# Kernel optimization log

Measured on AMD Instinct MI355X. Metric: run time of the kernel, lower is better.

## Reference

```python
import jax, jax.numpy as jnp
import numpy as np

B, L, D = 2, 2048, 2048
H, HKV, HD = 16, 4, 128
GROUPS = H // HKV


def _rope_tables(key):
    # standard RoPE cos/sin tables, shape (B, L, HD)
    inv_freq = 1.0 / (10000.0 ** (jnp.arange(0, HD, 2, dtype=jnp.float32) / HD))
    pos = jnp.arange(L, dtype=jnp.float32)
    freqs = pos[:, None] * inv_freq[None, :]          # (L, HD/2)
    emb = jnp.concatenate([freqs, freqs], axis=-1)    # (L, HD)
    cos = jnp.broadcast_to(jnp.cos(emb)[None], (B, L, HD))
    sin = jnp.broadcast_to(jnp.sin(emb)[None], (B, L, HD))
    return cos, sin


def setup_inputs() -> dict:
    key = jax.random.key(0)
    ks = jax.random.split(key, 5)
    x = jax.random.normal(ks[0], (B, L, D), dtype=jnp.float32)
    cos, sin = _rope_tables(ks[1])
    s = 1.0 / np.sqrt(D)
    Wq = jax.random.normal(ks[2], (D, D), dtype=jnp.float32) * s
    bq = jnp.zeros((D,), dtype=jnp.float32)
    Wkv = jax.random.normal(ks[3], (2 * HKV * HD, D), dtype=jnp.float32) * s
    bkv = jnp.zeros((2 * HKV * HD,), dtype=jnp.float32)
    Wo = jax.random.normal(ks[4], (D, D), dtype=jnp.float32) * s
    bo = jnp.zeros((D,), dtype=jnp.float32)
    return {"x": x, "cos": cos, "sin": sin, "Wq": Wq, "bq": bq,
            "Wkv": Wkv, "bkv": bkv, "Wo": Wo, "bo": bo}


def _rotate_half(t):
    t1, t2 = jnp.split(t, 2, axis=-1)
    return jnp.concatenate([-t2, t1], axis=-1)


def reference(x, cos, sin, Wq, bq, Wkv, bkv, Wo, bo):
    b, l, d = x.shape
    # QKV projections
    q = (x @ Wq.T + bq).reshape(b, l, H, HD)
    kv = (x @ Wkv.T + bkv).reshape(b, l, 2, HKV, HD)
    k, v = kv[:, :, 0], kv[:, :, 1]
    # RoPE (unsqueeze over head dim, layout B,L,H,D)
    c = cos[:, :, None, :]
    s = sin[:, :, None, :]
    q = q * c + _rotate_half(q) * s
    k = k * c + _rotate_half(k) * s
    # GQA: expand kv heads to query heads
    k = jnp.repeat(k, GROUPS, axis=2)
    v = jnp.repeat(v, GROUPS, axis=2)
    # causal attention (flash_attn_func equivalent math)
    scores = jnp.einsum("blhd,bmhd->bhlm", q, k) / jnp.sqrt(jnp.float32(HD))
    mask = jnp.tril(jnp.ones((l, l), dtype=bool))
    scores = jnp.where(mask[None, None], scores, jnp.finfo(scores.dtype).min)
    attn = jax.nn.softmax(scores, axis=-1)
    out = jnp.einsum("bhlm,bmhd->blhd", attn, v).reshape(b, l, H * HD)
    return out @ Wo.T + bo
```

## Files before the change

kernel.cpp:

```cpp
#include <hip/hip_runtime.h>
#include <hip/hip_bf16.h>
#include <cstddef>

constexpr int B = 2, L = 2048, D = 2048;
constexpr int H = 16, HKV = 4, HD = 128;
constexpr int GROUPS = H / HKV;
constexpr int KVD = 2 * HKV * HD;
constexpr int M_ROWS = B * L;
constexpr int QKVW = D + KVD;

typedef __attribute__((ext_vector_type(8))) short short8;
typedef __attribute__((ext_vector_type(4))) short s16x4;
typedef __attribute__((ext_vector_type(4))) float f32x4;

__device__ __forceinline__ short f2bf(float f) {
    union { float f; unsigned u; } v; v.f = f;
    unsigned r = v.u + 0x7FFFu + ((v.u >> 16) & 1u);
    return (short)(r >> 16);
}

__device__ __forceinline__ float fast_exp2(float x) {
#if __has_builtin(__builtin_amdgcn_exp2f)
    return __builtin_amdgcn_exp2f(x);
#else
    return exp2f(x);
#endif
}

__device__ __forceinline__ int invp(int pos) {
    const int b16 = pos >> 4, j = pos & 15;
    return ((b16 >> 1) << 4) + j + ((b16 & 1) << 6);
}

typedef __attribute__((address_space(1))) const void cg_void;
typedef __attribute__((address_space(3))) void lds_void;
__device__ __forceinline__ void gl_lds16(const void* g, void* l) {
    __builtin_amdgcn_global_load_lds((cg_void*)g, (lds_void*)l, 16, 0, 0);
}

__global__ __launch_bounds__(256) void cast_all(
    const float* __restrict__ x, const float* __restrict__ Wq,
    const float* __restrict__ Wkv, const float* __restrict__ Wo,
    short* __restrict__ xb, short* __restrict__ wqkvb, short* __restrict__ wob)
{
    constexpr int n_x   = M_ROWS * D / 4;
    constexpr int n_wq  = D * D / 4;
    constexpr int n_wkv = KVD * D / 4;
    constexpr int RPW   = D / 4;
    int i = blockIdx.x * 256 + threadIdx.x;
    const float* src; short* dst; int isrc;
    if (i < n_x) {
        src = x; dst = xb; isrc = i;
    } else if (i < n_x + n_wq) {
        i -= n_x; src = Wq; dst = wqkvb;
        const int fi = i / RPW, col = i % RPW;
        const int head = fi >> 7, pos = fi & 127;
        isrc = ((head << 7) + invp(pos)) * RPW + col;
    } else if (i < n_x + n_wq + n_wkv) {
        i -= n_x + n_wq; src = Wkv; dst = wqkvb + (size_t)D * D;
        const int fi = i / RPW, col = i % RPW;
        if (fi < HKV * HD) {
            isrc = (((fi >> 7) << 7) + invp(fi & 127)) * RPW + col;
        } else {
            isrc = i;
        }
    } else {
        i -= n_x + n_wq + n_wkv; src = Wo; dst = wob; isrc = i;
    }
    const float4 f = ((const float4*)src)[isrc];
    s16x4 s;
    s[0] = f2bf(f.x); s[1] = f2bf(f.y); s[2] = f2bf(f.z); s[3] = f2bf(f.w);
    ((s16x4*)dst)[i] = s;
}

__global__ __launch_bounds__(256) void bcat(
    const float* __restrict__ bq, const float* __restrict__ bkv, float* __restrict__ o)
{
    const int i = blockIdx.x * 256 + threadIdx.x;
    float v;
    if (i < D)                  v = bq[((i >> 7) << 7) + invp(i & 127)];
    else if (i < D + HKV * HD)  v = bkv[(((i - D) >> 7) << 7) + invp((i - D) & 127)];
    else                        v = bkv[i - D];
    o[i] = v;
}

template<int MODE>
__global__ __launch_bounds__(512, 2) void gemm256(
    const short* __restrict__ Ag, const short* __restrict__ Wg,
    const float* __restrict__ bias, float* __restrict__ C,
    const float* __restrict__ cosp, const float* __restrict__ sinp,
    short* __restrict__ qout, short* __restrict__ kout, short* __restrict__ vtout,
    int M, int N, int K)
{
    __shared__ __align__(1024) char smem[131072];

    const int tid = threadIdx.x;
    const int w = tid >> 6, lane = tid & 63;
    const int quad = lane >> 4, n16 = lane & 15;
    const int wr = w >> 2, wc = w & 3;

    const int nbx = gridDim.x;
    const int nwg = nbx * gridDim.y;
    int wg = blockIdx.y * nbx + blockIdx.x;
    wg = (wg & 7) * (nwg >> 3) + (wg >> 3);
    const int bm = (wg / nbx) << 8;
    const int bn = (wg % nbx) << 8;

    const int nkt = K >> 6;

    const int sbo = n16 * 64 + ((quad * 16) ^ ((n16 & 8) << 2));

    const int srow = lane >> 2;
    const int scol = ((lane & 3) * 8) ^ (((lane >> 5) & 1) << 4);

    f32x4 acc[8][4];
#pragma unroll
    for (int i = 0; i < 8; ++i)
#pragma unroll
        for (int j = 0; j < 4; ++j)
#pragma unroll
            for (int r = 0; r < 4; ++r) acc[i][j][r] = 0.f;

    short8 afr[4][2], bfr[2][2];

#define STAGE_A(k0, cb, h)                                                     \
    { _Pragma("unroll") for (int j = 0; j < 2; ++j) {                          \
        const int s  = w + j * 8;                                              \
        const int u  = s >> 1;                                                 \
        const int rg = ((u >> 2) << 3) + ((h) << 2) + (u & 3);                 \
        const int gr = bm + (rg << 4) + srow;                                  \
        const int gc = (k0) + ((s & 1) << 5) + scol;                           \
        gl_lds16(Ag + (size_t)gr * K + gc,                                     \
                 smem + (cb) * 32768 + (h) * 16384 + (s << 10)); } }

#define STAGE_B(k0, cb, h)                                                     \
    { _Pragma("unroll") for (int j = 0; j < 2; ++j) {                          \
        const int s  = w + j * 8;                                              \
        const int u  = s >> 1;                                                 \
        const int rg = ((u >> 1) << 2) + ((h) << 1) + (u & 1);                 \
        const int gr = bn + (rg << 4) + srow;                                  \
        const int gc = (k0) + ((s & 1) << 5) + scol;                           \
        gl_lds16(Wg + (size_t)gr * K + gc,                                     \
                 smem + 65536 + (cb) * 32768 + (h) * 16384 + (s << 10)); } }

#define PHASE(CB, Q, STAGE_STMT, WAIT_STMT)                                    \
    {                                                                          \
        if (((Q) & 1) == 0) {                                                  \
            _Pragma("unroll") for (int mi2 = 0; mi2 < 4; ++mi2)                \
            _Pragma("unroll") for (int kk = 0; kk < 2; ++kk)                   \
                afr[mi2][kk] = *(const short8*)(smem + (CB) * 32768 +          \
                    ((Q) >> 1) * 16384 +                                       \
                    ((((wr * 4 + mi2) * 2) + kk) << 10) + sbo);                \
        }                                                                      \
        _Pragma("unroll") for (int ni2 = 0; ni2 < 2; ++ni2)                    \
        _Pragma("unroll") for (int kk = 0; kk < 2; ++kk)                       \
            bfr[ni2][kk] = *(const short8*)(smem + 65536 + (CB) * 32768 +      \
                ((Q) & 1) * 16384 +                                            \
                ((((wc * 2 + ni2) * 2) + kk) << 10) + sbo);                    \
        STAGE_STMT;                                                            \
        WAIT_STMT;                                                             \
        __builtin_amdgcn_s_barrier();                                          \
        asm volatile("s_waitcnt lgkmcnt(0)" ::: "memory");                     \
        __builtin_amdgcn_sched_barrier(0);                                     \
        __builtin_amdgcn_s_setprio(1);                                         \
        _Pragma("unroll") for (int mi2 = 0; mi2 < 4; ++mi2)                    \
        _Pragma("unroll") for (int ni2 = 0; ni2 < 2; ++ni2)                    \
        _Pragma("unroll") for (int kk = 0; kk < 2; ++kk)                       \
            acc[((Q) >> 1) * 4 + mi2][((Q) & 1) * 2 + ni2] =                   \
                __builtin_amdgcn_mfma_f32_16x16x32_bf16(                       \
                    afr[mi2][kk], bfr[ni2][kk],                                \
                    acc[((Q) >> 1) * 4 + mi2][((Q) & 1) * 2 + ni2], 0, 0, 0);  \
        __builtin_amdgcn_s_setprio(0);                                         \
        asm volatile("" ::: "memory");                                         \
        __builtin_amdgcn_s_barrier();                                          \
    }

#define NOP_WAIT asm volatile("" ::: "memory")

    STAGE_A(0, 0, 0);
    STAGE_B(0, 0, 0);
    STAGE_A(0, 0, 1);
    STAGE_B(0, 0, 1);
    if (nkt > 1) {
        STAGE_A(64, 1, 0);
        STAGE_B(64, 1, 0);
    }
    asm volatile("s_waitcnt vmcnt(4)" ::: "memory");
    __builtin_amdgcn_s_barrier();

    for (int t = 0; t < nkt; t += 2) {
        const int k1 = (t + 1) << 6, k2 = (t + 2) << 6, k3 = (t + 3) << 6;
        const bool g2 = (t + 2) < nkt, g3 = (t + 3) < nkt;

        PHASE(0, 0, { STAGE_A(k1, 1, 1); }, NOP_WAIT);
        PHASE(0, 1, { STAGE_B(k1, 1, 1); }, NOP_WAIT);
        PHASE(0, 2, { if (g2) STAGE_A(k2, 0, 0); }, NOP_WAIT);
        PHASE(0, 3, { if (g2) STAGE_B(k2, 0, 0); },
              { if (g2) asm volatile("s_waitcnt vmcnt(4)" ::: "memory");
                else    asm volatile("s_waitcnt vmcnt(0)" ::: "memory"); });

        PHASE(1, 0, { if (g2) STAGE_A(k2, 0, 1); }, NOP_WAIT);
        PHASE(1, 1, { if (g2) STAGE_B(k2, 0, 1); }, NOP_WAIT);
        PHASE(1, 2, { if (g3) STAGE_A(k3, 1, 0); }, NOP_WAIT);
        PHASE(1, 3, { if (g3) STAGE_B(k3, 1, 0); },
              { if (g3) asm volatile("s_waitcnt vmcnt(4)" ::: "memory");
                else    asm volatile("s_waitcnt vmcnt(0)" ::: "memory"); });
    }

#undef PHASE
#undef STAGE_A
#undef STAGE_B
#undef NOP_WAIT

    if (MODE == 0) {
#pragma unroll
        for (int mh = 0; mh < 2; ++mh)
#pragma unroll
            for (int mi2 = 0; mi2 < 4; ++mi2)
#pragma unroll
                for (int r = 0; r < 4; ++r) {
                    const int row = bm + wr * 128 + mh * 64 + mi2 * 16 + quad * 4 + r;
#pragma unroll
                    for (int nh = 0; nh < 2; ++nh)
#pragma unroll
                        for (int ni2 = 0; ni2 < 2; ++ni2) {
                            const int col = bn + wc * 64 + nh * 32 + ni2 * 16 + n16;
                            C[(size_t)row * N + col] =
                                acc[mh * 4 + mi2][nh * 2 + ni2][r] + bias[col];
                        }
                }
    } else {
        short* const T = (short*)smem;
        __syncthreads();
        if (bn < D + HKV * HD) {
#pragma unroll
            for (int mh = 0; mh < 2; ++mh)
#pragma unroll
                for (int mi2 = 0; mi2 < 4; ++mi2)
#pragma unroll
                    for (int r = 0; r < 4; ++r) {
                        const int rl = wr * 128 + mh * 64 + mi2 * 16 + quad * 4 + r;
                        const int row = bm + rl;
                        const float* csrow = cosp + (size_t)row * HD;
                        const float* snrow = sinp + (size_t)row * HD;
                        const int sw = ((rl >> 2) & 7) << 4;
#pragma unroll
                        for (int nh = 0; nh < 2; ++nh) {
                            const int cl = wc * 64 + nh * 32 + n16;
                            const int iif = (wc & 1) * 32 + nh * 16 + n16;
                            const float a  = acc[mh * 4 + mi2][nh * 2 + 0][r] + bias[bn + cl];
                            const float bb = acc[mh * 4 + mi2][nh * 2 + 1][r] + bias[bn + cl + 16];
                            const float olo = a * csrow[iif]       - bb * snrow[iif];
                            const float ohi = bb * csrow[iif + 64] + a * snrow[iif + 64];
                            *(short*)((char*)T + ((rl * 512 + cl * 2) ^ sw))        = f2bf(olo);
                            *(short*)((char*)T + ((rl * 512 + (cl + 16) * 2) ^ sw)) = f2bf(ohi);
                        }
                    }
            __syncthreads();
            const bool isK = (bn >= D);
#pragma unroll
            for (int it = 0; it < 16; ++it) {
                const int idx = it * 512 + tid;
                const int rl = idx >> 5, c8 = idx & 31;
                const short8 v = *(const short8*)((char*)T +
                    ((rl * 512 + c8 * 16) ^ (((rl >> 2) & 7) << 4)));
                const int row = bm + rl;
                if (!isK) {
                    *(short8*)&qout[(size_t)row * D + bn + c8 * 8] = v;
                } else {
                    const int ck = bn - D + c8 * 8;
                    const int hk = ck >> 7, dk = ck & 127;
                    const int b_ = row >> 11, l_ = row & (L - 1);
                    *(short8*)&kout[((size_t)(b_ * HKV + hk) * L + l_) * HD + dk] = v;
                }
            }
        } else {
#pragma unroll
            for (int mh = 0; mh < 2; ++mh)
#pragma unroll
                for (int mi2 = 0; mi2 < 4; ++mi2) {
                    const int l0 = wr * 128 + mh * 64 + mi2 * 16 + quad * 4;
#pragma unroll
                    for (int nh = 0; nh < 2; ++nh)
#pragma unroll
                        for (int ni2 = 0; ni2 < 2; ++ni2) {
                            const int cl = wc * 64 + nh * 32 + ni2 * 16 + n16;
                            const float bs = bias[bn + cl];
                            s16x4 sv;
#pragma unroll
                            for (int r = 0; r < 4; ++r)
                                sv[r] = f2bf(acc[mh * 4 + mi2][nh * 2 + ni2][r] + bs);
                            *(s16x4*)((char*)T + ((cl * 512 + l0 * 2) ^ ((cl & 7) << 4))) = sv;
                        }
                }
            __syncthreads();
#pragma unroll
            for (int it = 0; it < 16; ++it) {
                const int idx = it * 512 + tid;
                const int cvr = idx >> 5, l8 = idx & 31;
                const short8 v = *(const short8*)((char*)T +
                    ((cvr * 512 + l8 * 16) ^ ((cvr & 7) << 4)));
                const int cv = bn - (D + HKV * HD) + cvr;
                const int hv = cv >> 7, dv = cv & 127;
                const int b_ = bm >> 11;
                const int lg = (bm & (L - 1)) + l8 * 8;
                *(short8*)&vtout[((size_t)(b_ * HKV + hv) * HD + dv) * L + lg] = v;
            }
        }
    }
}

__global__ __launch_bounds__(512) void attn_mfma4(
    const short* __restrict__ qb_, const short* __restrict__ kb_,
    const short* __restrict__ vtb_, short* __restrict__ ob)
{
    __shared__ __align__(16) char smem[86016];
    short* const KsB  = (short*)smem;
    short* const VtB  = (short*)(smem + 32768);
    short* const PbB  = (short*)(smem + 65536);
    float* const Rbuf = (float*)smem;

    const int hkv = blockIdx.y, b = blockIdx.z;
    const int tid = threadIdx.x;
    const int w = tid >> 6, lane = tid & 63;
    const int quad = lane >> 4, n16 = lane & 15;
    const int h   = hkv * GROUPS + (w & 3);
    const int kh  = (w >> 2) * 32;
    const int khg = (w >> 2) * 4;

    const size_t kbase  = (size_t)(b * HKV + hkv) * L * HD;
    const size_t vtbase = (size_t)(b * HKV + hkv) * HD * L;
    const float c1 = 0.12751845f;
    const float c0 = -28.853901f;

    short8 ones;
#pragma unroll
    for (int i = 0; i < 8; ++i) ones[i] = (short)0x3F80;

    const int kr = lane >> 4;
    const int kg_sw = lane & 15;
    const int vr = lane >> 3;
    const int vg_sw = lane & 7;

    short* const myPb = PbB + w * (2 * 16 * 40);

#pragma unroll 1
    for (int phase = 0; phase < 2; ++phase) {
        const int qidx = phase ? (63 - (int)blockIdx.x) : (int)blockIdx.x;
        const int qb0 = qidx * 32;
        const int ntiles = (qidx >> 1) + 1;

        short8 qf[2][4];
#pragma unroll
        for (int rt = 0; rt < 2; ++rt)
#pragma unroll
            for (int kk = 0; kk < 4; ++kk)
                qf[rt][kk] = *(const short8*)&qb_[
                    ((size_t)(b * L + qb0 + rt * 16 + n16)) * D + h * HD + kk * 32 + quad * 8];

        f32x4 oacc[2][8], lacc[2];
#pragma unroll
        for (int rt = 0; rt < 2; ++rt) {
#pragma unroll
            for (int r = 0; r < 4; ++r) lacc[rt][r] = 0.f;
#pragma unroll
            for (int nt = 0; nt < 8; ++nt)
#pragma unroll
                for (int r = 0; r < 4; ++r) oacc[rt][nt][r] = 0.f;
        }

        __syncthreads();

        {
            const short* kg = kb_ + kbase;
            const short* vg = vtb_ + vtbase;
#pragma unroll
            for (int j = 0; j < 2; ++j) {
                const int chunk = w * 2 + j;
                const int r = chunk * 4 + kr;
                gl_lds16(kg + r * HD + (kg_sw ^ (r & 15)) * 8, KsB + chunk * 512);
            }
#pragma unroll
            for (int j = 0; j < 2; ++j) {
                const int chunk = w * 2 + j;
                const int d = chunk * 8 + vr;
                gl_lds16(vg + (size_t)d * L + (vg_sw ^ (d & 7)) * 8, VtB + chunk * 512);
            }
        }

        for (int kt = 0; kt < ntiles; ++kt) {
            const int buf = kt & 1;
            __syncthreads();

            if (kt + 1 < ntiles) {
                const short* kg = kb_ + kbase + (size_t)((kt + 1) * 64) * HD;
                const short* vg = vtb_ + vtbase + (kt + 1) * 64;
#pragma unroll
                for (int j = 0; j < 2; ++j) {
                    const int chunk = w * 2 + j;
                    const int r = chunk * 4 + kr;
                    gl_lds16(kg + r * HD + (kg_sw ^ (r & 15)) * 8,
                             KsB + (buf ^ 1) * 8192 + chunk * 512);
                }
#pragma unroll
                for (int j = 0; j < 2; ++j) {
                    const int chunk = w * 2 + j;
                    const int d = chunk * 8 + vr;
                    gl_lds16(vg + (size_t)d * L + (vg_sw ^ (d & 7)) * 8,
                             VtB + (buf ^ 1) * 8192 + chunk * 512);
                }
            }

            const short* Ks = KsB + buf * 8192;
            const short* Vt = VtB + buf * 8192;

            f32x4 s[2][2];
#pragma unroll
            for (int rt = 0; rt < 2; ++rt)
#pragma unroll
                for (int ktl = 0; ktl < 2; ++ktl)
#pragma unroll
                    for (int r = 0; r < 4; ++r) s[rt][ktl][r] = 0.f;
#pragma unroll
            for (int kk = 0; kk < 4; ++kk) {
                short8 kf[2];
#pragma unroll
                for (int ktl = 0; ktl < 2; ++ktl) {
                    const int row = kh + ktl * 16 + n16;
                    kf[ktl] = *(const short8*)&Ks[row * 128 + ((kk * 4 + quad) ^ n16) * 8];
                }
#pragma unroll
                for (int rt = 0; rt < 2; ++rt)
#pragma unroll
                    for (int ktl = 0; ktl < 2; ++ktl)
                        s[rt][ktl] = __builtin_amdgcn_mfma_f32_16x16x32_bf16(
                            qf[rt][kk], kf[ktl], s[rt][ktl], 0, 0, 0);
            }

            const bool lastt = (kt == ntiles - 1);
#pragma unroll
            for (int rt = 0; rt < 2; ++rt) {
#pragma unroll
                for (int ktl = 0; ktl < 2; ++ktl) {
                    const int key0 = kt * 64 + kh + ktl * 16 + n16;
#pragma unroll
                    for (int r = 0; r < 4; ++r) {
                        float sv = s[rt][ktl][r];
                        if (lastt) {
                            const int qi = qb0 + rt * 16 + quad * 4 + r;
                            sv = (key0 <= qi) ? sv : -1e30f;
                        }
                        const float e = fast_exp2(sv * c1 + c0);
                        myPb[(rt * 16 + quad * 4 + r) * 40 + ktl * 16 + n16] = f2bf(e);
                    }
                }
            }
            asm volatile("s_waitcnt lgkmcnt(0)" ::: "memory");

            short8 pf[2];
#pragma unroll
            for (int rt = 0; rt < 2; ++rt)
                pf[rt] = *(const short8*)&myPb[(rt * 16 + n16) * 40 + quad * 8];
#pragma unroll
            for (int rt = 0; rt < 2; ++rt)
                lacc[rt] = __builtin_amdgcn_mfma_f32_16x16x32_bf16(pf[rt], ones, lacc[rt], 0, 0, 0);
#pragma unroll
            for (int nt = 0; nt < 8; ++nt) {
                const short8 vf = *(const short8*)&Vt[
                    (nt * 16 + n16) * 64 + ((khg + quad) ^ (n16 & 7)) * 8];
#pragma unroll
                for (int rt = 0; rt < 2; ++rt)
                    oacc[rt][nt] = __builtin_amdgcn_mfma_f32_16x16x32_bf16(pf[rt], vf, oacc[rt][nt], 0, 0, 0);
            }
        }

        __syncthreads();
        if (w >= 4) {
            float* rp = Rbuf + ((size_t)(w - 4) * 64 + lane) * 76;
#pragma unroll
            for (int rt = 0; rt < 2; ++rt)
#pragma unroll
                for (int nt = 0; nt < 8; ++nt)
                    *(f32x4*)&rp[(rt * 8 + nt) * 4] = oacc[rt][nt];
            *(f32x4*)&rp[64] = lacc[0];
            *(f32x4*)&rp[68] = lacc[1];
        }
        __syncthreads();
        if (w < 4) {
            const float* rp = Rbuf + ((size_t)w * 64 + lane) * 76;
#pragma unroll
            for (int rt = 0; rt < 2; ++rt) {
                const f32x4 lr = *(const f32x4*)&rp[64 + rt * 4];
#pragma unroll
                for (int r = 0; r < 4; ++r) lacc[rt][r] += lr[r];
#pragma unroll
                for (int nt = 0; nt < 8; ++nt) {
                    const f32x4 o2 = *(const f32x4*)&rp[(rt * 8 + nt) * 4];
#pragma unroll
                    for (int r = 0; r < 4; ++r) oacc[rt][nt][r] += o2[r];
                }
            }
#pragma unroll
            for (int rt = 0; rt < 2; ++rt) {
#pragma unroll
                for (int r = 0; r < 4; ++r) {
                    const float inv = 1.0f / lacc[rt][r];
                    short* op = ob + ((size_t)(b * L + qb0 + rt * 16 + quad * 4 + r)) * D + h * HD + n16;
#pragma unroll
                    for (int nt = 0; nt < 8; ++nt) op[nt * 16] = f2bf(oacc[rt][nt][r] * inv);
                }
            }
        }
    }
}

extern "C" void kernel_launch(void* const* d_in, const int* in_sizes, int n_in,
                              void* d_out, int out_size, void* d_ws, size_t ws_size,
                              hipStream_t stream)
{
    const float* x    = (const float*)d_in[0];
    const float* cosp = (const float*)d_in[1];
    const float* sinp = (const float*)d_in[2];
    const float* Wq   = (const float*)d_in[3];
    const float* bq   = (const float*)d_in[4];
    const float* Wkv  = (const float*)d_in[5];
    const float* bkv  = (const float*)d_in[6];
    const float* Wo   = (const float*)d_in[7];
    const float* bo   = (const float*)d_in[8];
    float* out = (float*)d_out;

    char* p = (char*)d_ws;
    short* x_bf    = (short*)p; p += (size_t)M_ROWS * D * 2;
    short* wqkv_bf = (short*)p; p += (size_t)QKVW * D * 2;
    short* wo_bf   = (short*)p; p += (size_t)D * D * 2;
    float* b_qkv   = (float*)p; p += (size_t)QKVW * 4;
    short* q_bf    = (short*)p; p += (size_t)M_ROWS * D * 2;
    short* k_bf    = (short*)p; p += (size_t)M_ROWS * HKV * HD * 2;
    short* vt_bf   = (short*)p;
    short* attn_bf = x_bf;

    dim3 blk(256);

    cast_all<<<dim3(18432), blk, 0, stream>>>(x, Wq, Wkv, Wo, x_bf, wqkv_bf, wo_bf);
    bcat<<<dim3(QKVW / 256), blk, 0, stream>>>(bq, bkv, b_qkv);

    gemm256<1><<<dim3(QKVW / 256, M_ROWS / 256), dim3(512), 0, stream>>>(
        x_bf, wqkv_bf, b_qkv, nullptr, cosp, sinp, q_bf, k_bf, vt_bf,
        M_ROWS, QKVW, D);

    attn_mfma4<<<dim3(32, HKV, B), dim3(512), 0, stream>>>(q_bf, k_bf, vt_bf, attn_bf);

    gemm256<0><<<dim3(D / 256, M_ROWS / 256), dim3(512), 0, stream>>>(
        attn_bf, wo_bf, bo, out, nullptr, nullptr, nullptr, nullptr, nullptr,
        M_ROWS, D, D);
}
```

Measured before the change: 303.1 us.

## Fold bias concat into cast kernel and halve GEMM phases per K-tile

The separate bias-concatenation kernel is removed and its work moved into extra threads of the cast kernel, saving one launch. The GEMM main loop drops from four phases per K-tile to two: each phase loads a full 4x4 fragment set (B fragments read once per tile), issues 32 MFMAs and stages A and B together. This halves barriers per tile and cuts redundant LDS reads, but uses more B-fragment registers and issues larger bursts of global loads at once, which can lower overlap or occupancy.

```diff
diff --git a/kernel.cpp b/kernel.cpp
--- a/kernel.cpp
+++ b/kernel.cpp
@@ -41,13 +41,32 @@
 __global__ __launch_bounds__(256) void cast_all(
     const float* __restrict__ x, const float* __restrict__ Wq,
     const float* __restrict__ Wkv, const float* __restrict__ Wo,
-    short* __restrict__ xb, short* __restrict__ wqkvb, short* __restrict__ wob)
+    const float* __restrict__ bq, const float* __restrict__ bkv,
+    short* __restrict__ xb, short* __restrict__ wqkvb, short* __restrict__ wob,
+    float* __restrict__ bqkv)
 {
     constexpr int n_x   = M_ROWS * D / 4;
     constexpr int n_wq  = D * D / 4;
     constexpr int n_wkv = KVD * D / 4;
+    constexpr int n_wo  = D * D / 4;
+    constexpr int n_w   = n_x + n_wq + n_wkv + n_wo;
     constexpr int RPW   = D / 4;
     int i = blockIdx.x * 256 + threadIdx.x;
+    if (i >= n_w) {
+        const int j = i - n_w;
+        float4 o;
+#pragma unroll
+        for (int e = 0; e < 4; ++e) {
+            const int idx = j * 4 + e;
+            float v;
+            if (idx < D)                 v = bq[((idx >> 7) << 7) + invp(idx & 127)];
+            else if (idx < D + HKV * HD) v = bkv[(((idx - D) >> 7) << 7) + invp((idx - D) & 127)];
+            else                         v = bkv[idx - D];
+            (&o.x)[e] = v;
+        }
+        ((float4*)bqkv)[j] = o;
+        return;
+    }
     const float* src; short* dst; int isrc;
     if (i < n_x) {
         src = x; dst = xb; isrc = i;
@@ -73,17 +92,6 @@
     ((s16x4*)dst)[i] = s;
 }
 
-__global__ __launch_bounds__(256) void bcat(
-    const float* __restrict__ bq, const float* __restrict__ bkv, float* __restrict__ o)
-{
-    const int i = blockIdx.x * 256 + threadIdx.x;
-    float v;
-    if (i < D)                  v = bq[((i >> 7) << 7) + invp(i & 127)];
-    else if (i < D + HKV * HD)  v = bkv[(((i - D) >> 7) << 7) + invp((i - D) & 127)];
-    else                        v = bkv[i - D];
-    o[i] = v;
-}
-
 template<int MODE>
 __global__ __launch_bounds__(512, 2) void gemm256(
     const short* __restrict__ Ag, const short* __restrict__ Wg,
@@ -121,7 +129,7 @@
 #pragma unroll
             for (int r = 0; r < 4; ++r) acc[i][j][r] = 0.f;
 
-    short8 afr[4][2], bfr[2][2];
+    short8 afr[4][2], bfr[4][2];
 
 #define STAGE_A(k0, cb, h)                                                     \
     { _Pragma("unroll") for (int j = 0; j < 2; ++j) {                          \
@@ -143,20 +151,19 @@
         gl_lds16(Wg + (size_t)gr * K + gc,                                     \
                  smem + 65536 + (cb) * 32768 + (h) * 16384 + (s << 10)); } }
 
-#define PHASE(CB, Q, STAGE_STMT, WAIT_STMT)                                    \
+#define PHASE(CB, MH, RDB, STAGE_STMT, WAIT_STMT)                              \
     {                                                                          \
-        if (((Q) & 1) == 0) {                                                  \
-            _Pragma("unroll") for (int mi2 = 0; mi2 < 4; ++mi2)                \
+        if (RDB) {                                                             \
+            _Pragma("unroll") for (int nj = 0; nj < 4; ++nj)                   \
             _Pragma("unroll") for (int kk = 0; kk < 2; ++kk)                   \
-                afr[mi2][kk] = *(const short8*)(smem + (CB) * 32768 +          \
-                    ((Q) >> 1) * 16384 +                                       \
-                    ((((wr * 4 + mi2) * 2) + kk) << 10) + sbo);                \
+                bfr[nj][kk] = *(const short8*)(smem + 65536 + (CB) * 32768 +   \
+                    (nj >> 1) * 16384 +                                        \
+                    ((((wc * 2 + (nj & 1)) * 2) + kk) << 10) + sbo);           \
         }                                                                      \
-        _Pragma("unroll") for (int ni2 = 0; ni2 < 2; ++ni2)                    \
+        _Pragma("unroll") for (int mi2 = 0; mi2 < 4; ++mi2)                    \
         _Pragma("unroll") for (int kk = 0; kk < 2; ++kk)                       \
-            bfr[ni2][kk] = *(const short8*)(smem + 65536 + (CB) * 32768 +      \
-                ((Q) & 1) * 16384 +                                            \
-                ((((wc * 2 + ni2) * 2) + kk) << 10) + sbo);                    \
+            afr[mi2][kk] = *(const short8*)(smem + (CB) * 32768 +              \
+                (MH) * 16384 + ((((wr * 4 + mi2) * 2) + kk) << 10) + sbo);     \
         STAGE_STMT;                                                            \
         WAIT_STMT;                                                             \
         __builtin_amdgcn_s_barrier();                                          \
@@ -164,12 +171,12 @@
         __builtin_amdgcn_sched_barrier(0);                                     \
         __builtin_amdgcn_s_setprio(1);                                         \
         _Pragma("unroll") for (int mi2 = 0; mi2 < 4; ++mi2)                    \
-        _Pragma("unroll") for (int ni2 = 0; ni2 < 2; ++ni2)                    \
+        _Pragma("unroll") for (int nj = 0; nj < 4; ++nj)                       \
         _Pragma("unroll") for (int kk = 0; kk < 2; ++kk)                       \
-            acc[((Q) >> 1) * 4 + mi2][((Q) & 1) * 2 + ni2] =                   \
+            acc[(MH) * 4 + mi2][nj] =                                          \
                 __builtin_amdgcn_mfma_f32_16x16x32_bf16(                       \
-                    afr[mi2][kk], bfr[ni2][kk],                                \
-                    acc[((Q) >> 1) * 4 + mi2][((Q) & 1) * 2 + ni2], 0, 0, 0);  \
+                    afr[mi2][kk], bfr[nj][kk], acc[(MH) * 4 + mi2][nj],        \
+                    0, 0, 0);                                                  \
         __builtin_amdgcn_s_setprio(0);                                         \
         asm volatile("" ::: "memory");                                         \
         __builtin_amdgcn_s_barrier();                                          \
@@ -184,25 +191,23 @@
     if (nkt > 1) {
         STAGE_A(64, 1, 0);
         STAGE_B(64, 1, 0);
-    }
-    asm volatile("s_waitcnt vmcnt(4)" ::: "memory");
+        asm volatile("s_waitcnt vmcnt(4)" ::: "memory");
+    } else {
+        asm volatile("s_waitcnt vmcnt(0)" ::: "memory");
+    }
     __builtin_amdgcn_s_barrier();
 
     for (int t = 0; t < nkt; t += 2) {
         const int k1 = (t + 1) << 6, k2 = (t + 2) << 6, k3 = (t + 3) << 6;
         const bool g2 = (t + 2) < nkt, g3 = (t + 3) < nkt;
 
-        PHASE(0, 0, { STAGE_A(k1, 1, 1); }, NOP_WAIT);
-        PHASE(0, 1, { STAGE_B(k1, 1, 1); }, NOP_WAIT);
-        PHASE(0, 2, { if (g2) STAGE_A(k2, 0, 0); }, NOP_WAIT);
-        PHASE(0, 3, { if (g2) STAGE_B(k2, 0, 0); },
+        PHASE(0, 0, 1, { STAGE_A(k1, 1, 1); STAGE_B(k1, 1, 1); }, NOP_WAIT);
+        PHASE(0, 1, 0, { if (g2) { STAGE_A(k2, 0, 0); STAGE_B(k2, 0, 0); } },
               { if (g2) asm volatile("s_waitcnt vmcnt(4)" ::: "memory");
                 else    asm volatile("s_waitcnt vmcnt(0)" ::: "memory"); });
 
-        PHASE(1, 0, { if (g2) STAGE_A(k2, 0, 1); }, NOP_WAIT);
-        PHASE(1, 1, { if (g2) STAGE_B(k2, 0, 1); }, NOP_WAIT);
-        PHASE(1, 2, { if (g3) STAGE_A(k3, 1, 0); }, NOP_WAIT);
-        PHASE(1, 3, { if (g3) STAGE_B(k3, 1, 0); },
+        PHASE(1, 0, 1, { if (g2) { STAGE_A(k2, 0, 1); STAGE_B(k2, 0, 1); } }, NOP_WAIT);
+        PHASE(1, 1, 0, { if (g3) { STAGE_A(k3, 1, 0); STAGE_B(k3, 1, 0); } },
               { if (g3) asm volatile("s_waitcnt vmcnt(4)" ::: "memory");
                 else    asm volatile("s_waitcnt vmcnt(0)" ::: "memory"); });
     }
@@ -541,8 +546,8 @@
 
     dim3 blk(256);
 
-    cast_all<<<dim3(18432), blk, 0, stream>>>(x, Wq, Wkv, Wo, x_bf, wqkv_bf, wo_bf);
-    bcat<<<dim3(QKVW / 256), blk, 0, stream>>>(bq, bkv, b_qkv);
+    cast_all<<<dim3(18435), blk, 0, stream>>>(
+        x, Wq, Wkv, Wo, bq, bkv, x_bf, wqkv_bf, wo_bf, b_qkv);
 
     gemm256<1><<<dim3(QKVW / 256, M_ROWS / 256), dim3(512), 0, stream>>>(
         x_bf, wqkv_bf, b_qkv, nullptr, cosp, sinp, q_bf, k_bf, vt_bf,
```

After: 298.3 us. Within noise of the previous version (-1.6%).
